# Kernel optimization log

Hardware: AMD Instinct MI355X
Metric: run time of the kernel (lower is better)

## Reference

```python
import jax, jax.numpy as jnp
import numpy as np

T = 64    # target_len
D = 256   # av_dim


def setup_inputs() -> dict:
    key = jax.random.key(0)
    ks = jax.random.split(key, 8)
    B, L = 128, 512
    return {
        "acoustic_seq": jax.random.normal(ks[0], (B, L, D), jnp.float32),
        "visual_seq": jax.random.normal(ks[1], (B, L, D), jnp.float32),
        "IS_BAG_list": jnp.ones((B, L), jnp.int32),
        # h_fc: Linear(target_len, target_len)
        "Wh": jax.random.normal(ks[2], (T, T), jnp.float32) * 0.05,
        "bh": jax.random.normal(ks[3], (T,), jnp.float32) * 0.05,
        # w_fc: Linear(av_dim, av_dim)
        "Ww": jax.random.normal(ks[4], (D, D), jnp.float32) * 0.05,
        "bw": jax.random.normal(ks[5], (D,), jnp.float32) * 0.05,
        # conv: Conv2d(2, 1, kernel_size=1) -> two scalars + bias
        "conv_w": jax.random.normal(ks[6], (2,), jnp.float32) * 0.5,
        "conv_b": jax.random.normal(ks[7], (1,), jnp.float32) * 0.1,
    }


def reference(acoustic_seq, visual_seq, IS_BAG_list, Wh, bh, Ww, bw, conv_w, conv_b):
    B, L, Dd = acoustic_seq.shape
    G = L // T  # uniform group size (deterministic variant of random group sizes)
    mapping = jnp.repeat(jnp.arange(T), G)  # [L] pooled-frame index per original frame

    # resize_sequence (m_len > target_len branch): group-mean pooling to T frames
    aco_p = acoustic_seq.reshape(B, T, G, Dd).mean(axis=2)  # [B,T,D]
    vis_p = visual_seq.reshape(B, T, G, Dd).mean(axis=2)    # [B,T,D]

    # c_attention = sigmoid(Conv2d(2->1, 1x1)(stack([aco,vis], ch)))
    c_att = jax.nn.sigmoid(conv_w[0] * aco_p + conv_w[1] * vis_p + conv_b[0])  # [B,T,D]

    # hw_attention = mean over channel dim
    hw = 0.5 * (aco_p + vis_p)                                 # [B,T,D]
    h_att = jax.nn.sigmoid(hw.mean(axis=2) @ Wh.T + bh)        # [B,T]
    w_att = jax.nn.sigmoid(hw.mean(axis=1) @ Ww.T + bw)        # [B,D]

    # recover_sequence (m_len > target_len): gather attention[mapping]
    h_full = h_att[:, mapping][..., None]   # [B,L,1]
    w_full = w_att[:, None, :]              # [B,1,D]
    c_full = c_att[:, mapping, :]           # [B,L,D]

    scale = (h_full + w_full + c_full) / 3.0
    mask = (IS_BAG_list == 1)[..., None]    # [B,L,1]
    aco_out = jnp.where(mask, acoustic_seq * scale, acoustic_seq)
    vis_out = jnp.where(mask, visual_seq * scale, visual_seq)
    return aco_out, vis_out
```

## Files before the change

kernel.cpp:

```cpp
#include <hip/hip_runtime.h>
#include <math.h>

#define BB 128
#define LL 512
#define DD 256
#define TT 64
#define GG 8

typedef float f32x4 __attribute__((ext_vector_type(4)));

__device__ __forceinline__ float sigm(float x) {
    return 1.0f / (1.0f + __expf(-x));
}

__global__ void k_pool(const f32x4* __restrict__ aco, const f32x4* __restrict__ vis,
                       const float* __restrict__ conv_w, const float* __restrict__ conv_b,
                       f32x4* __restrict__ c_att, f32x4* __restrict__ hw_buf,
                       float* __restrict__ hwRowMean)
{
    const int tid = threadIdx.x;
    const int q   = tid & 63;
    const int r   = tid >> 6;
    const int bt  = blockIdx.x * 4 + r;
    const int b   = bt >> 6;
    const int t   = bt & 63;

    size_t base = ((size_t)(b * LL + t * GG)) * (DD / 4) + q;
    f32x4 sa = 0.f, sv = 0.f;
#pragma unroll
    for (int g = 0; g < GG; ++g) {
        sa += aco[base + (size_t)g * (DD / 4)];
        sv += vis[base + (size_t)g * (DD / 4)];
    }
    sa *= 0.125f;
    sv *= 0.125f;

    const float cw0 = conv_w[0], cw1 = conv_w[1], cb = conv_b[0];
    f32x4 z  = cw0 * sa + cw1 * sv + cb;
    f32x4 ca;
    ca.x = sigm(z.x); ca.y = sigm(z.y); ca.z = sigm(z.z); ca.w = sigm(z.w);
    f32x4 hw = 0.5f * (sa + sv);

    c_att[(size_t)bt * (DD / 4) + q]  = ca;
    hw_buf[(size_t)bt * (DD / 4) + q] = hw;

    float hsum = hw.x + hw.y + hw.z + hw.w;
#pragma unroll
    for (int off = 32; off > 0; off >>= 1)
        hsum += __shfl_xor(hsum, off, 64);
    if (q == 0) hwRowMean[bt] = hsum * (1.0f / DD);
}

__global__ void k_gates(const float* __restrict__ hw_buf, const float* __restrict__ hwRowMean,
                        const float* __restrict__ Wh, const float* __restrict__ bh,
                        const float* __restrict__ Ww, const float* __restrict__ bw,
                        float* __restrict__ h_att, float* __restrict__ w_att)
{
    const int b = blockIdx.x;
    const int d = threadIdx.x;

    __shared__ float row[TT];
    __shared__ float cm[DD];

    if (d < TT) row[d] = hwRowMean[b * TT + d];

    float s = 0.f;
    const float* hb = hw_buf + (size_t)b * TT * DD + d;
#pragma unroll
    for (int t = 0; t < TT; ++t) s += hb[(size_t)t * DD];
    cm[d] = s * (1.0f / TT);
    __syncthreads();

    if (d < TT) {
        float acc = bh[d];
#pragma unroll
        for (int j = 0; j < TT; ++j) acc += row[j] * Wh[d * TT + j];
        h_att[b * TT + d] = sigm(acc);
    }

    float acc = bw[d];
    const float* wr = Ww + (size_t)d * DD;
#pragma unroll 4
    for (int k = 0; k < DD; k += 4) {
        f32x4 w4 = *reinterpret_cast<const f32x4*>(wr + k);
        acc += cm[k] * w4.x + cm[k + 1] * w4.y + cm[k + 2] * w4.z + cm[k + 3] * w4.w;
    }
    w_att[b * DD + d] = sigm(acc);
}

__global__ void k_apply(const f32x4* __restrict__ aco, const f32x4* __restrict__ vis,
                        const int* __restrict__ isbag,
                        const f32x4* __restrict__ c_att, const float* __restrict__ h_att,
                        const f32x4* __restrict__ w_att,
                        f32x4* __restrict__ out)
{
    const size_t N4 = (size_t)BB * LL * DD / 4;
    const size_t stride = (size_t)gridDim.x * blockDim.x;
    for (size_t i = (size_t)blockIdx.x * blockDim.x + threadIdx.x; i < N4; i += stride) {
        const int row = (int)(i >> 6);
        const int dq  = (int)(i & 63);
        const int b   = row >> 9;
        const int l   = row & 511;
        const int t   = l >> 3;

        const float h  = h_att[b * TT + t];
        const f32x4 w4 = w_att[b * (DD / 4) + dq];
        const f32x4 c4 = c_att[((size_t)(b * TT + t)) * (DD / 4) + dq];
        const bool  m  = (isbag[row] == 1);

        f32x4 a4 = aco[i];
        f32x4 v4 = vis[i];
        f32x4 s4 = (h + w4 + c4) * (1.0f / 3.0f);

        f32x4 oa = m ? (f32x4)(a4 * s4) : a4;
        f32x4 ov = m ? (f32x4)(v4 * s4) : v4;

        __builtin_nontemporal_store(oa, &out[i]);
        __builtin_nontemporal_store(ov, &out[N4 + i]);
    }
}

extern "C" void kernel_launch(void* const* d_in, const int* in_sizes, int n_in,
                              void* d_out, int out_size, void* d_ws, size_t ws_size,
                              hipStream_t stream) {
    const float* aco = (const float*)d_in[0];
    const float* vis = (const float*)d_in[1];
    const int*   isb = (const int*)d_in[2];
    const float* Wh  = (const float*)d_in[3];
    const float* bh  = (const float*)d_in[4];
    const float* Ww  = (const float*)d_in[5];
    const float* bw  = (const float*)d_in[6];
    const float* cw  = (const float*)d_in[7];
    const float* cb  = (const float*)d_in[8];
    float* out = (float*)d_out;

    float* ws = (float*)d_ws;
    float* c_att     = ws;
    float* hw_buf    = c_att  + (size_t)BB * TT * DD;
    float* hwRowMean = hw_buf + (size_t)BB * TT * DD;
    float* h_att     = hwRowMean + BB * TT;
    float* w_att     = h_att + BB * TT;

    k_pool<<<BB * TT / 4, 256, 0, stream>>>(
        (const f32x4*)aco, (const f32x4*)vis, cw, cb,
        (f32x4*)c_att, (f32x4*)hw_buf, hwRowMean);

    k_gates<<<BB, DD, 0, stream>>>(hw_buf, hwRowMean, Wh, bh, Ww, bw, h_att, w_att);

    k_apply<<<2048, 256, 0, stream>>>(
        (const f32x4*)aco, (const f32x4*)vis, isb,
        (const f32x4*)c_att, h_att, (const f32x4*)w_att,
        (f32x4*)out);
}
```

Baseline: 82.02 us.

## Fuse pool, gates and apply into one cooperative kernel with grid sync

Replaces the three-kernel pipeline with a single cooperative kernel. Each block pools its 64 rows and writes row means and partial column sums. After a grid-wide sync it computes the gates and scales the outputs. The acoustic tile stays in registers and LDS, so it is read from HBM once, while the visual tile is read twice. Intermediate c_att/hw buffers and two launches disappear. In exchange, 1024 blocks must be co-resident, and there is a grid-sync barrier plus high register and LDS pressure. A fallback to the old path runs if the cooperative launch fails.

```diff
diff --git a/kernel.cpp b/kernel.cpp
--- a/kernel.cpp
+++ b/kernel.cpp
@@ -1,16 +1,165 @@
 #include <hip/hip_runtime.h>
+#include <hip/hip_cooperative_groups.h>
 #include <math.h>
+
+namespace cg = cooperative_groups;
 
 #define BB 128
 #define LL 512
 #define DD 256
 #define TT 64
 #define GG 8
+#define NQ (DD/4)
 
 typedef float f32x4 __attribute__((ext_vector_type(4)));
 
 __device__ __forceinline__ float sigm(float x) {
     return 1.0f / (1.0f + __expf(-x));
+}
+__device__ __forceinline__ f32x4 sigm4(f32x4 z) {
+    f32x4 r;
+    r.x = sigm(z.x); r.y = sigm(z.y); r.z = sigm(z.z); r.w = sigm(z.w);
+    return r;
+}
+
+__global__ __launch_bounds__(256, 4) void k_fused(
+    const f32x4* __restrict__ aco4, const f32x4* __restrict__ vis4,
+    const int* __restrict__ isb,
+    const float* __restrict__ Wh, const float* __restrict__ bh,
+    const float* __restrict__ Ww, const float* __restrict__ bw,
+    const float* __restrict__ cw, const float* __restrict__ cb,
+    f32x4* __restrict__ out4,
+    float* __restrict__ rowMean,
+    float* __restrict__ colpart)
+{
+    cg::grid_group grid = cg::this_grid();
+
+    __shared__ f32x4 acoL[4 * 8 * 64];
+    __shared__ __align__(16) float red[4 * DD];
+
+    const int tid  = threadIdx.x;
+    const int w    = tid >> 6;
+    const int lane = tid & 63;
+    const int bk   = blockIdx.x;
+    const int b    = bk >> 3;
+    const int t8   = bk & 7;
+
+    const size_t rowBase = (size_t)b * LL + (size_t)t8 * 64 + (size_t)w * 16;
+    const size_t N4 = (size_t)BB * LL * NQ;
+
+    f32x4 A[8];
+    f32x4 pa0 = 0.f;
+#pragma unroll
+    for (int j = 0; j < 8; ++j) {
+        A[j] = aco4[(rowBase + j) * NQ + lane];
+        pa0 += A[j];
+    }
+    f32x4 pa1 = 0.f;
+#pragma unroll
+    for (int j = 0; j < 8; ++j) {
+        f32x4 v = aco4[(rowBase + 8 + j) * NQ + lane];
+        acoL[(w * 8 + j) * 64 + lane] = v;
+        pa1 += v;
+    }
+    f32x4 pv0 = 0.f, pv1 = 0.f;
+#pragma unroll
+    for (int j = 0; j < 8; ++j) pv0 += vis4[(rowBase + j) * NQ + lane];
+#pragma unroll
+    for (int j = 0; j < 8; ++j) pv1 += vis4[(rowBase + 8 + j) * NQ + lane];
+
+    pa0 *= 0.125f; pa1 *= 0.125f; pv0 *= 0.125f; pv1 *= 0.125f;
+
+    const float cw0 = cw[0], cw1 = cw[1], cb0 = cb[0];
+    const f32x4 c0 = sigm4(cw0 * pa0 + cw1 * pv0 + cb0);
+    const f32x4 c1 = sigm4(cw0 * pa1 + cw1 * pv1 + cb0);
+    const f32x4 hw0 = 0.5f * (pa0 + pv0);
+    const f32x4 hw1 = 0.5f * (pa1 + pv1);
+
+    float s0 = hw0.x + hw0.y + hw0.z + hw0.w;
+    float s1 = hw1.x + hw1.y + hw1.z + hw1.w;
+#pragma unroll
+    for (int off = 32; off > 0; off >>= 1) {
+        s0 += __shfl_xor(s0, off, 64);
+        s1 += __shfl_xor(s1, off, 64);
+    }
+    if (lane == 0) {
+        const int btBase = b * TT + t8 * 8 + 2 * w;
+        rowMean[btBase]     = s0 * (1.0f / DD);
+        rowMean[btBase + 1] = s1 * (1.0f / DD);
+    }
+
+    *reinterpret_cast<f32x4*>(&red[w * DD + lane * 4]) = hw0 + hw1;
+    __syncthreads();
+    colpart[(size_t)bk * DD + tid] =
+        red[tid] + red[DD + tid] + red[2 * DD + tid] + red[3 * DD + tid];
+
+    grid.sync();
+
+    float* cm = red;
+    float* wv = red + DD;
+    float* rm = red + 2 * DD;
+    float* hv = red + 2 * DD + TT;
+
+    {
+        float cs = 0.f;
+#pragma unroll
+        for (int p = 0; p < 8; ++p)
+            cs += colpart[(size_t)(b * 8 + p) * DD + tid];
+        cm[tid] = cs * (1.0f / TT);
+        if (tid < TT) rm[tid] = rowMean[b * TT + tid];
+    }
+    __syncthreads();
+
+    if (tid < 8) {
+        const int t = t8 * 8 + tid;
+        float acc = bh[t];
+#pragma unroll 8
+        for (int j = 0; j < TT; ++j) acc += rm[j] * Wh[t * TT + j];
+        hv[tid] = sigm(acc);
+    }
+    {
+        float acc = bw[tid];
+        const f32x4* Wr = reinterpret_cast<const f32x4*>(Ww + (size_t)tid * DD);
+#pragma unroll 8
+        for (int kq = 0; kq < NQ; ++kq) {
+            f32x4 wq = Wr[kq];
+            acc += cm[4 * kq] * wq.x + cm[4 * kq + 1] * wq.y +
+                   cm[4 * kq + 2] * wq.z + cm[4 * kq + 3] * wq.w;
+        }
+        wv[tid] = sigm(acc);
+    }
+    __syncthreads();
+
+    const float hA = hv[2 * w];
+    const float hB = hv[2 * w + 1];
+    f32x4 w4;
+    w4.x = wv[lane * 4]; w4.y = wv[lane * 4 + 1];
+    w4.z = wv[lane * 4 + 2]; w4.w = wv[lane * 4 + 3];
+    const f32x4 scA = (hA + w4 + c0) * (1.0f / 3.0f);
+    const f32x4 scB = (hB + w4 + c1) * (1.0f / 3.0f);
+
+#pragma unroll
+    for (int j = 0; j < 8; ++j) {
+        const size_t ridx = rowBase + j;
+        const size_t idx  = ridx * NQ + lane;
+        const int m = isb[ridx];
+        f32x4 a = A[j];
+        f32x4 v = vis4[idx];
+        if (m == 1) { a *= scA; v *= scA; }
+        __builtin_nontemporal_store(a, &out4[idx]);
+        __builtin_nontemporal_store(v, &out4[N4 + idx]);
+    }
+#pragma unroll
+    for (int j = 0; j < 8; ++j) {
+        const size_t ridx = rowBase + 8 + j;
+        const size_t idx  = ridx * NQ + lane;
+        const int m = isb[ridx];
+        f32x4 a = acoL[(w * 8 + j) * 64 + lane];
+        f32x4 v = vis4[idx];
+        if (m == 1) { a *= scB; v *= scB; }
+        __builtin_nontemporal_store(a, &out4[idx]);
+        __builtin_nontemporal_store(v, &out4[N4 + idx]);
+    }
 }
 
 __global__ void k_pool(const f32x4* __restrict__ aco, const f32x4* __restrict__ vis,
@@ -25,24 +174,22 @@
     const int b   = bt >> 6;
     const int t   = bt & 63;
 
-    size_t base = ((size_t)(b * LL + t * GG)) * (DD / 4) + q;
+    size_t base = ((size_t)(b * LL + t * GG)) * NQ + q;
     f32x4 sa = 0.f, sv = 0.f;
 #pragma unroll
     for (int g = 0; g < GG; ++g) {
-        sa += aco[base + (size_t)g * (DD / 4)];
-        sv += vis[base + (size_t)g * (DD / 4)];
+        sa += aco[base + (size_t)g * NQ];
+        sv += vis[base + (size_t)g * NQ];
     }
     sa *= 0.125f;
     sv *= 0.125f;
 
     const float cw0 = conv_w[0], cw1 = conv_w[1], cb = conv_b[0];
-    f32x4 z  = cw0 * sa + cw1 * sv + cb;
-    f32x4 ca;
-    ca.x = sigm(z.x); ca.y = sigm(z.y); ca.z = sigm(z.z); ca.w = sigm(z.w);
+    f32x4 ca = sigm4(cw0 * sa + cw1 * sv + cb);
     f32x4 hw = 0.5f * (sa + sv);
 
-    c_att[(size_t)bt * (DD / 4) + q]  = ca;
-    hw_buf[(size_t)bt * (DD / 4) + q] = hw;
+    c_att[(size_t)bt * NQ + q]  = ca;
+    hw_buf[(size_t)bt * NQ + q] = hw;
 
     float hsum = hw.x + hw.y + hw.z + hw.w;
 #pragma unroll
@@ -94,7 +241,7 @@
                         const f32x4* __restrict__ w_att,
                         f32x4* __restrict__ out)
 {
-    const size_t N4 = (size_t)BB * LL * DD / 4;
+    const size_t N4 = (size_t)BB * LL * NQ;
     const size_t stride = (size_t)gridDim.x * blockDim.x;
     for (size_t i = (size_t)blockIdx.x * blockDim.x + threadIdx.x; i < N4; i += stride) {
         const int row = (int)(i >> 6);
@@ -104,8 +251,8 @@
         const int t   = l >> 3;
 
         const float h  = h_att[b * TT + t];
-        const f32x4 w4 = w_att[b * (DD / 4) + dq];
-        const f32x4 c4 = c_att[((size_t)(b * TT + t)) * (DD / 4) + dq];
+        const f32x4 w4 = w_att[b * NQ + dq];
+        const f32x4 c4 = c_att[((size_t)(b * TT + t)) * NQ + dq];
         const bool  m  = (isbag[row] == 1);
 
         f32x4 a4 = aco[i];
@@ -123,8 +270,8 @@
 extern "C" void kernel_launch(void* const* d_in, const int* in_sizes, int n_in,
                               void* d_out, int out_size, void* d_ws, size_t ws_size,
                               hipStream_t stream) {
-    const float* aco = (const float*)d_in[0];
-    const float* vis = (const float*)d_in[1];
+    const f32x4* aco = (const f32x4*)d_in[0];
+    const f32x4* vis = (const f32x4*)d_in[1];
     const int*   isb = (const int*)d_in[2];
     const float* Wh  = (const float*)d_in[3];
     const float* bh  = (const float*)d_in[4];
@@ -132,23 +279,34 @@
     const float* bw  = (const float*)d_in[6];
     const float* cw  = (const float*)d_in[7];
     const float* cb  = (const float*)d_in[8];
-    float* out = (float*)d_out;
+    f32x4* out = (f32x4*)d_out;
 
     float* ws = (float*)d_ws;
-    float* c_att     = ws;
+    float* rowMean = ws;
+    float* colpart = ws + BB * TT;
+    float* fb        = ws + BB * TT + 1024 * DD;
+    float* c_att     = fb;
     float* hw_buf    = c_att  + (size_t)BB * TT * DD;
     float* hwRowMean = hw_buf + (size_t)BB * TT * DD;
     float* h_att     = hwRowMean + BB * TT;
     float* w_att     = h_att + BB * TT;
 
-    k_pool<<<BB * TT / 4, 256, 0, stream>>>(
-        (const f32x4*)aco, (const f32x4*)vis, cw, cb,
-        (f32x4*)c_att, (f32x4*)hw_buf, hwRowMean);
-
-    k_gates<<<BB, DD, 0, stream>>>(hw_buf, hwRowMean, Wh, bh, Ww, bw, h_att, w_att);
-
-    k_apply<<<2048, 256, 0, stream>>>(
-        (const f32x4*)aco, (const f32x4*)vis, isb,
-        (const f32x4*)c_att, h_att, (const f32x4*)w_att,
-        (f32x4*)out);
-}
+    void* kp[] = {
+        (void*)&aco, (void*)&vis, (void*)&isb,
+        (void*)&Wh, (void*)&bh, (void*)&Ww, (void*)&bw,
+        (void*)&cw, (void*)&cb, (void*)&out,
+        (void*)&rowMean, (void*)&colpart
+    };
+    hipError_t rc = hipLaunchCooperativeKernel((const void*)k_fused,
+                                               dim3(1024), dim3(256),
+                                               kp, 0, stream);
+    if (rc != hipSuccess) {
+        (void)hipGetLastError();
+        k_pool<<<BB * TT / 4, 256, 0, stream>>>(aco, vis, cw, cb,
+                                                (f32x4*)c_att, (f32x4*)hw_buf, hwRowMean);
+        k_gates<<<BB, DD, 0, stream>>>(hw_buf, hwRowMean, Wh, bh, Ww, bw, h_att, w_att);
+        k_apply<<<2048, 256, 0, stream>>>(aco, vis, isb,
+                                          (const f32x4*)c_att, h_att, (const f32x4*)w_att,
+                                          out);
+    }
+}
```

Result: slower. 200.8 us (+144.8%).

## Recompute pooled conv attention in apply kernel and drop large intermediate buffers

Applied to the files above, without the earlier changes.

The pooling kernel no longer writes the per-group conv attention and hw buffers. It now emits only row means and per-block column partial sums for the gate kernel. The apply kernel has each block own one pooled frame: it loads the 8 source rows, pools them through shared memory and recomputes the sigmoid conv attention locally. This removes a large workspace write and read in exchange for a shared-memory reduction and a barrier in the apply kernel.

```diff
diff --git a/kernel.cpp b/kernel.cpp
--- a/kernel.cpp
+++ b/kernel.cpp
@@ -6,125 +6,157 @@
 #define DD 256
 #define TT 64
 #define GG 8
+#define NQ (DD/4)
 
 typedef float f32x4 __attribute__((ext_vector_type(4)));
 
 __device__ __forceinline__ float sigm(float x) {
     return 1.0f / (1.0f + __expf(-x));
 }
-
-__global__ void k_pool(const f32x4* __restrict__ aco, const f32x4* __restrict__ vis,
-                       const float* __restrict__ conv_w, const float* __restrict__ conv_b,
-                       f32x4* __restrict__ c_att, f32x4* __restrict__ hw_buf,
-                       float* __restrict__ hwRowMean)
-{
-    const int tid = threadIdx.x;
-    const int q   = tid & 63;
-    const int r   = tid >> 6;
-    const int bt  = blockIdx.x * 4 + r;
-    const int b   = bt >> 6;
-    const int t   = bt & 63;
-
-    size_t base = ((size_t)(b * LL + t * GG)) * (DD / 4) + q;
-    f32x4 sa = 0.f, sv = 0.f;
-#pragma unroll
-    for (int g = 0; g < GG; ++g) {
-        sa += aco[base + (size_t)g * (DD / 4)];
-        sv += vis[base + (size_t)g * (DD / 4)];
-    }
-    sa *= 0.125f;
-    sv *= 0.125f;
-
-    const float cw0 = conv_w[0], cw1 = conv_w[1], cb = conv_b[0];
-    f32x4 z  = cw0 * sa + cw1 * sv + cb;
-    f32x4 ca;
-    ca.x = sigm(z.x); ca.y = sigm(z.y); ca.z = sigm(z.z); ca.w = sigm(z.w);
-    f32x4 hw = 0.5f * (sa + sv);
-
-    c_att[(size_t)bt * (DD / 4) + q]  = ca;
-    hw_buf[(size_t)bt * (DD / 4) + q] = hw;
-
-    float hsum = hw.x + hw.y + hw.z + hw.w;
-#pragma unroll
-    for (int off = 32; off > 0; off >>= 1)
-        hsum += __shfl_xor(hsum, off, 64);
-    if (q == 0) hwRowMean[bt] = hsum * (1.0f / DD);
+__device__ __forceinline__ f32x4 sigm4(f32x4 z) {
+    f32x4 r;
+    r.x = sigm(z.x); r.y = sigm(z.y); r.z = sigm(z.z); r.w = sigm(z.w);
+    return r;
 }
 
-__global__ void k_gates(const float* __restrict__ hw_buf, const float* __restrict__ hwRowMean,
-                        const float* __restrict__ Wh, const float* __restrict__ bh,
-                        const float* __restrict__ Ww, const float* __restrict__ bw,
-                        float* __restrict__ h_att, float* __restrict__ w_att)
+__global__ __launch_bounds__(256) void k_sum(
+    const f32x4* __restrict__ aco4, const f32x4* __restrict__ vis4,
+    float* __restrict__ rowMean,
+    float* __restrict__ colpart)
+{
+    const int tid  = threadIdx.x;
+    const int w    = tid >> 6;
+    const int lane = tid & 63;
+    const int bk   = blockIdx.x;
+    const int b    = bk >> 3;
+    const int t8   = bk & 7;
+
+    const size_t rowBase = (size_t)b * LL + (size_t)t8 * 64 + (size_t)w * 16;
+
+    f32x4 hw0 = 0.f, hw1 = 0.f;
+#pragma unroll
+    for (int j = 0; j < 8; ++j)
+        hw0 += aco4[(rowBase + j) * NQ + lane] + vis4[(rowBase + j) * NQ + lane];
+#pragma unroll
+    for (int j = 0; j < 8; ++j)
+        hw1 += aco4[(rowBase + 8 + j) * NQ + lane] + vis4[(rowBase + 8 + j) * NQ + lane];
+    hw0 *= 0.0625f;
+    hw1 *= 0.0625f;
+
+    float s0 = hw0.x + hw0.y + hw0.z + hw0.w;
+    float s1 = hw1.x + hw1.y + hw1.z + hw1.w;
+#pragma unroll
+    for (int off = 32; off > 0; off >>= 1) {
+        s0 += __shfl_xor(s0, off, 64);
+        s1 += __shfl_xor(s1, off, 64);
+    }
+    if (lane == 0) {
+        const int btBase = b * TT + t8 * 8 + 2 * w;
+        rowMean[btBase]     = s0 * (1.0f / DD);
+        rowMean[btBase + 1] = s1 * (1.0f / DD);
+    }
+
+    __shared__ __align__(16) float red[4][DD];
+    *reinterpret_cast<f32x4*>(&red[w][lane * 4]) = hw0 + hw1;
+    __syncthreads();
+    colpart[(size_t)bk * DD + tid] =
+        red[0][tid] + red[1][tid] + red[2][tid] + red[3][tid];
+}
+
+__global__ __launch_bounds__(256) void k_gates(
+    const float* __restrict__ colpart, const float* __restrict__ rowMean,
+    const float* __restrict__ Wh, const float* __restrict__ bh,
+    const float* __restrict__ Ww, const float* __restrict__ bw,
+    float* __restrict__ h_att, float* __restrict__ w_att)
 {
     const int b = blockIdx.x;
     const int d = threadIdx.x;
 
-    __shared__ float row[TT];
+    __shared__ float rm[TT];
     __shared__ float cm[DD];
 
-    if (d < TT) row[d] = hwRowMean[b * TT + d];
-
-    float s = 0.f;
-    const float* hb = hw_buf + (size_t)b * TT * DD + d;
+    {
+        float cs = 0.f;
 #pragma unroll
-    for (int t = 0; t < TT; ++t) s += hb[(size_t)t * DD];
-    cm[d] = s * (1.0f / TT);
+        for (int p = 0; p < 8; ++p)
+            cs += colpart[(size_t)(b * 8 + p) * DD + d];
+        cm[d] = cs * (1.0f / TT);
+        if (d < TT) rm[d] = rowMean[b * TT + d];
+    }
     __syncthreads();
 
     if (d < TT) {
         float acc = bh[d];
-#pragma unroll
-        for (int j = 0; j < TT; ++j) acc += row[j] * Wh[d * TT + j];
+#pragma unroll 8
+        for (int j = 0; j < TT; ++j) acc += rm[j] * Wh[d * TT + j];
         h_att[b * TT + d] = sigm(acc);
     }
-
-    float acc = bw[d];
-    const float* wr = Ww + (size_t)d * DD;
-#pragma unroll 4
-    for (int k = 0; k < DD; k += 4) {
-        f32x4 w4 = *reinterpret_cast<const f32x4*>(wr + k);
-        acc += cm[k] * w4.x + cm[k + 1] * w4.y + cm[k + 2] * w4.z + cm[k + 3] * w4.w;
+    {
+        float acc = bw[d];
+        const f32x4* Wr = reinterpret_cast<const f32x4*>(Ww + (size_t)d * DD);
+#pragma unroll 8
+        for (int kq = 0; kq < NQ; ++kq) {
+            f32x4 wq = Wr[kq];
+            acc += cm[4 * kq] * wq.x + cm[4 * kq + 1] * wq.y +
+                   cm[4 * kq + 2] * wq.z + cm[4 * kq + 3] * wq.w;
+        }
+        w_att[b * DD + d] = sigm(acc);
     }
-    w_att[b * DD + d] = sigm(acc);
 }
 
-__global__ void k_apply(const f32x4* __restrict__ aco, const f32x4* __restrict__ vis,
-                        const int* __restrict__ isbag,
-                        const f32x4* __restrict__ c_att, const float* __restrict__ h_att,
-                        const f32x4* __restrict__ w_att,
-                        f32x4* __restrict__ out)
+__global__ __launch_bounds__(256) void k_apply(
+    const f32x4* __restrict__ aco4, const f32x4* __restrict__ vis4,
+    const int* __restrict__ isb,
+    const float* __restrict__ h_att, const float* __restrict__ w_att,
+    const float* __restrict__ cw, const float* __restrict__ cb,
+    f32x4* __restrict__ out4)
 {
-    const size_t N4 = (size_t)BB * LL * DD / 4;
-    const size_t stride = (size_t)gridDim.x * blockDim.x;
-    for (size_t i = (size_t)blockIdx.x * blockDim.x + threadIdx.x; i < N4; i += stride) {
-        const int row = (int)(i >> 6);
-        const int dq  = (int)(i & 63);
-        const int b   = row >> 9;
-        const int l   = row & 511;
-        const int t   = l >> 3;
+    const int tid = threadIdx.x;
+    const int r   = tid >> 6;
+    const int q   = tid & 63;
+    const int bk  = blockIdx.x;
+    const int b   = bk >> 6;
+    const int t   = bk & 63;
 
-        const float h  = h_att[b * TT + t];
-        const f32x4 w4 = w_att[b * (DD / 4) + dq];
-        const f32x4 c4 = c_att[((size_t)(b * TT + t)) * (DD / 4) + dq];
-        const bool  m  = (isbag[row] == 1);
+    const size_t row0 = (size_t)b * LL + (size_t)t * GG + r;
+    const size_t N4   = (size_t)BB * LL * NQ;
 
-        f32x4 a4 = aco[i];
-        f32x4 v4 = vis[i];
-        f32x4 s4 = (h + w4 + c4) * (1.0f / 3.0f);
+    const size_t i0 = row0 * NQ + q;
+    const size_t i1 = (row0 + 4) * NQ + q;
 
-        f32x4 oa = m ? (f32x4)(a4 * s4) : a4;
-        f32x4 ov = m ? (f32x4)(v4 * s4) : v4;
+    f32x4 a0 = aco4[i0], a1 = aco4[i1];
+    f32x4 v0 = vis4[i0], v1 = vis4[i1];
 
-        __builtin_nontemporal_store(oa, &out[i]);
-        __builtin_nontemporal_store(ov, &out[N4 + i]);
-    }
+    __shared__ __align__(16) f32x4 redA[4][64];
+    __shared__ __align__(16) f32x4 redV[4][64];
+    redA[r][q] = a0 + a1;
+    redV[r][q] = v0 + v1;
+    __syncthreads();
+
+    const f32x4 pa = (redA[0][q] + redA[1][q] + redA[2][q] + redA[3][q]) * 0.125f;
+    const f32x4 pv = (redV[0][q] + redV[1][q] + redV[2][q] + redV[3][q]) * 0.125f;
+
+    const f32x4 c  = sigm4(cw[0] * pa + cw[1] * pv + cb[0]);
+    const float h  = h_att[b * TT + t];
+    const f32x4 w4 = *reinterpret_cast<const f32x4*>(w_att + (size_t)b * DD + q * 4);
+    const f32x4 sc = (h + w4 + c) * (1.0f / 3.0f);
+
+    const int m0 = isb[row0];
+    const int m1 = isb[row0 + 4];
+    if (m0 == 1) { a0 *= sc; v0 *= sc; }
+    if (m1 == 1) { a1 *= sc; v1 *= sc; }
+
+    __builtin_nontemporal_store(a0, &out4[i0]);
+    __builtin_nontemporal_store(a1, &out4[i1]);
+    __builtin_nontemporal_store(v0, &out4[N4 + i0]);
+    __builtin_nontemporal_store(v1, &out4[N4 + i1]);
 }
 
 extern "C" void kernel_launch(void* const* d_in, const int* in_sizes, int n_in,
                               void* d_out, int out_size, void* d_ws, size_t ws_size,
                               hipStream_t stream) {
-    const float* aco = (const float*)d_in[0];
-    const float* vis = (const float*)d_in[1];
+    const f32x4* aco = (const f32x4*)d_in[0];
+    const f32x4* vis = (const f32x4*)d_in[1];
     const int*   isb = (const int*)d_in[2];
     const float* Wh  = (const float*)d_in[3];
     const float* bh  = (const float*)d_in[4];
@@ -132,23 +164,15 @@
     const float* bw  = (const float*)d_in[6];
     const float* cw  = (const float*)d_in[7];
     const float* cb  = (const float*)d_in[8];
-    float* out = (float*)d_out;
+    f32x4* out = (f32x4*)d_out;
 
     float* ws = (float*)d_ws;
-    float* c_att     = ws;
-    float* hw_buf    = c_att  + (size_t)BB * TT * DD;
-    float* hwRowMean = hw_buf + (size_t)BB * TT * DD;
-    float* h_att     = hwRowMean + BB * TT;
-    float* w_att     = h_att + BB * TT;
+    float* rowMean = ws;
+    float* colpart = rowMean + BB * TT;
+    float* h_att   = colpart + 1024 * DD;
+    float* w_att   = h_att + BB * TT;
 
-    k_pool<<<BB * TT / 4, 256, 0, stream>>>(
-        (const f32x4*)aco, (const f32x4*)vis, cw, cb,
-        (f32x4*)c_att, (f32x4*)hw_buf, hwRowMean);
-
-    k_gates<<<BB, DD, 0, stream>>>(hw_buf, hwRowMean, Wh, bh, Ww, bw, h_att, w_att);
-
-    k_apply<<<2048, 256, 0, stream>>>(
-        (const f32x4*)aco, (const f32x4*)vis, isb,
-        (const f32x4*)c_att, h_att, (const f32x4*)w_att,
-        (f32x4*)out);
+    k_sum<<<1024, 256, 0, stream>>>(aco, vis, rowMean, colpart);
+    k_gates<<<BB, 256, 0, stream>>>(colpart, rowMean, Wh, bh, Ww, bw, h_att, w_att);
+    k_apply<<<BB * TT, 256, 0, stream>>>(aco, vis, isb, h_att, w_att, cw, cb, out);
 }
```

Result: faster. 76.15 us (median of 2 runs) (-7.2%).
